# Performance work log

Hardware: AMD Instinct MI355X
Metric: run time of the kernel (lower is better)

Reference implementation:

```python
import jax, jax.numpy as jnp
import numpy as np

B, L, D, H, R = 2, 128, 256, 8, 4
DK = D // H  # 32
EPS = 1e-6


def setup_inputs() -> dict:
    key = jax.random.key(0)
    ks = jax.random.split(key, 12)
    q = jax.random.normal(ks[0], (B, L, D), jnp.float32)
    k = jax.random.normal(ks[1], (B, L, D), jnp.float32)
    v = jax.random.normal(ks[2], (B, L, D), jnp.float32)
    t = jnp.sort(jax.random.uniform(ks[3], (B, L), jnp.float32), axis=-1)
    omega = jax.random.uniform(ks[4], (B, L, L), jnp.float32)
    mask = jnp.triu(jnp.ones((L, L), bool), 1)  # True = masked (causal)
    xav = (2.0 / (D + D)) ** 0.5
    Wq = jax.random.normal(ks[5], (D, H * DK), jnp.float32) * xav
    Wk = jax.random.normal(ks[6], (D, H * DK), jnp.float32) * xav
    Wv = jax.random.normal(ks[7], (D, H * DK), jnp.float32) * xav
    s = jax.random.uniform(ks[8], (R,), jnp.float32) + 0.1  # ODE time-decay scales
    fc_w = jax.random.normal(ks[9], (H * DK, D), jnp.float32) * xav
    fc_b = jnp.zeros((D,), jnp.float32)
    ln_g = jnp.ones((D,), jnp.float32)
    ln_b = jnp.zeros((D,), jnp.float32)
    return {"q": q, "k": k, "v": v, "t": t, "omega": omega, "mask": mask,
            "Wq": Wq, "Wk": Wk, "Wv": Wv, "s": s,
            "fc_w": fc_w, "fc_b": fc_b, "ln_g": ln_g, "ln_b": ln_b}


def _ode_proj(x, W, phi):
    # x: (B,L,D), W: (D,H*DK), phi: (B,L,L,R) time kernel
    p = x @ W                                       # (B,L,H*DK)
    y = p[:, None, :, None, :] * phi[..., None]     # (B,L,L,R,H*DK)
    y = y.reshape(B, L, L, R, H, DK)
    return y.transpose(0, 4, 1, 2, 3, 5)            # (B,H,L,L,R,DK)


def reference(q, k, v, t, omega, mask, Wq, Wk, Wv, s, fc_w, fc_b, ln_g, ln_b):
    temp = DK ** 0.5
    residual = q
    # pre-LayerNorm on q (normalize_before=True)
    mu = q.mean(-1, keepdims=True)
    var = q.var(-1, keepdims=True)
    qn = (q - mu) / jnp.sqrt(var + EPS) * ln_g + ln_b
    # continuous-time kernel phi[b,i,j,r] = exp(-|t_i - t_j| * s_r)
    dt = jnp.abs(t[:, :, None] - t[:, None, :])     # (B,L,L)
    phi = jnp.exp(-dt[..., None] * s)               # (B,L,L,R)
    q6 = _ode_proj(qn, Wq, phi)                     # (B,H,L,L,R,DK)
    k6 = _ode_proj(k, Wk, phi)
    v6 = _ode_proj(v, Wv, phi)
    # attn = (q/temp * k * omega).sum(-1).sum(-1)
    attn = jnp.einsum('bhijrd,bhijrd,bij->bhij', q6 / temp, k6, omega)
    attn = jnp.where(mask[None, None, :, :], -1e9, attn)
    attn = jax.nn.softmax(attn, axis=-1)            # (B,H,L,L)
    vsum = v6.sum(axis=4)                           # sum over R -> (B,H,L,L,DK)
    out = jnp.einsum('bhij,bhijd->bhid', attn, vsum)  # (B,H,L,DK)
    out = out.transpose(0, 2, 1, 3).reshape(B, L, H * DK)
    out = out @ fc_w + fc_b + residual              # dropout = identity (eval)
    return (out, attn)
```

## Files before the change

kernel.cpp:

```cpp
#include <hip/hip_runtime.h>

#define B_  2
#define L_  128
#define D_  256
#define H_  8
#define R_  4
#define DK_ 32
#define BL_ (B_*L_)
#define SXP 260

__device__ __forceinline__ float wredsum64(float v) {
    #pragma unroll
    for (int m = 32; m >= 1; m >>= 1) v += __shfl_xor(v, m, 64);
    return v;
}
__device__ __forceinline__ float wredmax64(float v) {
    #pragma unroll
    for (int m = 32; m >= 1; m >>= 1) v = fmaxf(v, __shfl_xor(v, m, 64));
    return v;
}

__global__ __launch_bounds__(256) void k_proj(
    const float* __restrict__ q, const float* __restrict__ k, const float* __restrict__ v,
    const float* __restrict__ Wq, const float* __restrict__ Wk, const float* __restrict__ Wv,
    const float* __restrict__ ln_g, const float* __restrict__ ln_b,
    float* __restrict__ pv, float* __restrict__ qkpart)
{
    const int blk = blockIdx.x;
    const int rowTile = blk >> 4;
    const int cg = blk & 15;
    const int rbase = rowTile * 4;
    const int tid = threadIdx.x;

    __shared__ __align__(16) float sx[3][4 * SXP];
    __shared__ __align__(16) float partF[16 * 4 * 16];
    __shared__ float spq[4][16], spk[4][16];

    {
        const int r = tid >> 6, f4c = tid & 63;
        #pragma unroll
        for (int p = 0; p < 3; ++p) {
            const float* src = (p == 0 ? q : (p == 1 ? k : v)) + (size_t)(rbase + r) * D_;
            *reinterpret_cast<float4*>(&sx[p][r * SXP + f4c * 4]) =
                reinterpret_cast<const float4*>(src)[f4c];
        }
    }
    __syncthreads();

    {
        const int r = tid >> 6, lane = tid & 63;
        float x0 = sx[0][r * SXP + lane];
        float x1 = sx[0][r * SXP + lane + 64];
        float x2 = sx[0][r * SXP + lane + 128];
        float x3 = sx[0][r * SXP + lane + 192];
        float s1 = x0 + x1 + x2 + x3;
        float s2 = x0*x0 + x1*x1 + x2*x2 + x3*x3;
        #pragma unroll
        for (int m = 32; m >= 1; m >>= 1) {
            s1 += __shfl_xor(s1, m, 64);
            s2 += __shfl_xor(s2, m, 64);
        }
        const float mu = s1 * (1.0f / D_);
        const float rs = rsqrtf(s2 * (1.0f / D_) - mu * mu + 1e-6f);
        sx[0][r * SXP + lane      ] = (x0 - mu) * rs * ln_g[lane      ] + ln_b[lane      ];
        sx[0][r * SXP + lane +  64] = (x1 - mu) * rs * ln_g[lane +  64] + ln_b[lane +  64];
        sx[0][r * SXP + lane + 128] = (x2 - mu) * rs * ln_g[lane + 128] + ln_b[lane + 128];
        sx[0][r * SXP + lane + 192] = (x3 - mu) * rs * ln_g[lane + 192] + ln_b[lane + 192];
    }
    __syncthreads();

    const int kg  = tid >> 4;
    const int row = (tid >> 2) & 3;
    const int c4  = tid & 3;
    const int gc4 = cg * 4 + c4;
    const int kbase = kg * 16;

    #pragma unroll
    for (int m = 0; m < 3; ++m) {
        const float4* W4 = reinterpret_cast<const float4*>(m == 0 ? Wq : (m == 1 ? Wk : Wv));
        float4 a = {0, 0, 0, 0};
        #pragma unroll
        for (int kk = 0; kk < 16; ++kk) {
            const int kr = kbase + kk;
            const float x = sx[m][row * SXP + kr];
            const float4 w = W4[kr * 64 + gc4];
            a.x += x * w.x; a.y += x * w.y; a.z += x * w.z; a.w += x * w.w;
        }
        *reinterpret_cast<float4*>(&partF[(kg * 16 + row * 4 + c4) * 4]) = a;
        __syncthreads();
        if (tid < 64) {
            const int rr = tid >> 4, cc = tid & 15;
            float sum = 0.f;
            #pragma unroll
            for (int g = 0; g < 16; ++g) sum += partF[g * 64 + rr * 16 + cc];
            if      (m == 0) spq[rr][cc] = sum;
            else if (m == 1) spk[rr][cc] = sum;
            else             pv[(size_t)(rbase + rr) * D_ + cg * 16 + cc] = sum;
        }
        __syncthreads();
    }

    if (tid < 64) {
        const int rr = tid >> 4, cc = tid & 15;
        float d = spq[rr][cc] * spk[rr][cc];
        #pragma unroll
        for (int m = 8; m >= 1; m >>= 1) d += __shfl_xor(d, m, 64);
        if (cc == 0) qkpart[(size_t)(rbase + rr) * 16 + cg] = d;
    }
}

__global__ __launch_bounds__(256) void k_attn(
    const float* __restrict__ t, const float* __restrict__ omega, const float* __restrict__ s,
    const float* __restrict__ pv, const float* __restrict__ qkpart,
    float* __restrict__ mid, float* __restrict__ dout)
{
    const int blk = blockIdx.x;
    const int b     = blk >> 8;
    const int itile = (blk >> 3) & 31;
    const int h     = blk & 7;
    const int ibase = itile * 4;
    const int tid = threadIdx.x;

    __shared__ __align__(16) float sQKp[L_ * 16];
    __shared__ __align__(16) float sQKh[L_];
    __shared__ __align__(16) float sOm[4 * L_];
    __shared__ __align__(16) float sPhi[4 * L_], sPsi[4 * L_];
    __shared__ __align__(16) float sAttn[4 * L_];
    __shared__ __align__(16) float partF[32 * 4 * 32];
    __shared__ float st[L_], sS[R_];

    {
        const float4* qkp4 = reinterpret_cast<const float4*>(qkpart + (size_t)b * L_ * 16);
        reinterpret_cast<float4*>(sQKp)[tid]       = qkp4[tid];
        reinterpret_cast<float4*>(sQKp)[tid + 256] = qkp4[tid + 256];
        if (tid < 128)
            reinterpret_cast<float4*>(sOm)[tid] =
                reinterpret_cast<const float4*>(omega + ((size_t)(b * L_ + ibase)) * L_)[tid];
        if (tid < 32)
            reinterpret_cast<float4*>(st)[tid] =
                reinterpret_cast<const float4*>(t + (size_t)b * L_)[tid];
        if (tid < R_) sS[tid] = s[tid];
    }
    __syncthreads();

    if (tid < 128) sQKh[tid] = sQKp[tid * 16 + 2 * h] + sQKp[tid * 16 + 2 * h + 1];
    #pragma unroll
    for (int p = 0; p < 2; ++p) {
        const int idx = tid + p * 256;
        const int w = idx >> 7, j = idx & 127;
        const float dtv = fabsf(st[ibase + w] - st[j]);
        float Phi = 0.f, Psi = 0.f;
        #pragma unroll
        for (int r = 0; r < R_; ++r) {
            const float e = expf(-dtv * sS[r]);
            Phi += e;
            Psi += e * e;
        }
        sPhi[idx] = Phi;
        sPsi[idx] = Psi;
    }
    __syncthreads();

    const int w = tid >> 6, lane = tid & 63;
    const int i = ibase + w;
    {
        const float invtemp = 0.17677669529663687f;
        const int j0 = lane, j1 = lane + 64;
        float l0 = (j0 <= i) ? sOm[w*L_ + j0] * sPsi[w*L_ + j0] * sQKh[j0] * invtemp : -3.0e38f;
        float l1 = (j1 <= i) ? sOm[w*L_ + j1] * sPsi[w*L_ + j1] * sQKh[j1] * invtemp : -3.0e38f;
        const float mx = wredmax64(fmaxf(l0, l1));
        const float e0 = (j0 <= i) ? expf(l0 - mx) : 0.f;
        const float e1 = (j1 <= i) ? expf(l1 - mx) : 0.f;
        const float inv = 1.0f / wredsum64(e0 + e1);
        const float a0 = e0 * inv, a1 = e1 * inv;
        sAttn[w*L_ + j0] = a0;
        sAttn[w*L_ + j1] = a1;
        const size_t ab = (size_t)BL_ * D_ + (((size_t)(b * H_ + h) * L_ + i) * L_);
        dout[ab + j0] = a0;
        dout[ab + j1] = a1;
    }
    __syncthreads();

    {
        const int jg = tid >> 3, c4 = tid & 7;
        const int gc4 = h * 8 + c4;
        const float4* pv4 = reinterpret_cast<const float4*>(pv + (size_t)b * L_ * D_);
        float4 acc[4];
        #pragma unroll
        for (int ww = 0; ww < 4; ++ww) acc[ww] = make_float4(0, 0, 0, 0);
        #pragma unroll
        for (int jj = 0; jj < 4; ++jj) {
            const int j = jg + jj * 32;
            const float4 p = pv4[j * 64 + gc4];
            #pragma unroll
            for (int ww = 0; ww < 4; ++ww) {
                const float wgt = sAttn[ww*L_ + j] * sPhi[ww*L_ + j];
                acc[ww].x += wgt * p.x; acc[ww].y += wgt * p.y;
                acc[ww].z += wgt * p.z; acc[ww].w += wgt * p.w;
            }
        }
        #pragma unroll
        for (int ww = 0; ww < 4; ++ww)
            *reinterpret_cast<float4*>(&partF[(jg * 32 + ww * 8 + c4) * 4]) = acc[ww];
    }
    __syncthreads();
    if (tid < 128) {
        const int ww = tid >> 5, cc = tid & 31;
        float sum = 0.f;
        #pragma unroll
        for (int g = 0; g < 32; ++g) sum += partF[g * 128 + ww * 32 + cc];
        mid[((size_t)(b * L_ + ibase + ww)) * D_ + h * 32 + cc] = sum;
    }
}

__global__ __launch_bounds__(256) void k_fc(
    const float* __restrict__ q, const float* __restrict__ fc_w, const float* __restrict__ fc_b,
    const float* __restrict__ mid, float* __restrict__ dout)
{
    const int blk = blockIdx.x;
    const int rowTile = blk >> 4;
    const int cg = blk & 15;
    const int rbase = rowTile * 4;
    const int tid = threadIdx.x;

    __shared__ __align__(16) float smid[4 * SXP];
    __shared__ __align__(16) float partF[16 * 4 * 16];

    {
        const int r = tid >> 6, f4c = tid & 63;
        *reinterpret_cast<float4*>(&smid[r * SXP + f4c * 4]) =
            reinterpret_cast<const float4*>(mid + (size_t)(rbase + r) * D_)[f4c];
    }
    __syncthreads();

    const int kg  = tid >> 4;
    const int row = (tid >> 2) & 3;
    const int c4  = tid & 3;
    const int gc4 = cg * 4 + c4;
    const int kbase = kg * 16;
    const float4* fw4 = reinterpret_cast<const float4*>(fc_w);
    float4 a = {0, 0, 0, 0};
    #pragma unroll
    for (int kk = 0; kk < 16; ++kk) {
        const int kr = kbase + kk;
        const float x = smid[row * SXP + kr];
        const float4 wv = fw4[kr * 64 + gc4];
        a.x += x * wv.x; a.y += x * wv.y; a.z += x * wv.z; a.w += x * wv.w;
    }
    *reinterpret_cast<float4*>(&partF[(kg * 16 + row * 4 + c4) * 4]) = a;
    __syncthreads();

    if (tid < 64) {
        const int rr = tid >> 4, cc = tid & 15;
        const int col = cg * 16 + cc;
        float sum = fc_b[col] + q[(size_t)(rbase + rr) * D_ + col];
        #pragma unroll
        for (int g = 0; g < 16; ++g) sum += partF[g * 64 + rr * 16 + cc];
        dout[(size_t)(rbase + rr) * D_ + col] = sum;
    }
}

extern "C" void kernel_launch(void* const* d_in, const int* in_sizes, int n_in,
                              void* d_out, int out_size, void* d_ws, size_t ws_size,
                              hipStream_t stream) {
    const float* q     = (const float*)d_in[0];
    const float* k     = (const float*)d_in[1];
    const float* v     = (const float*)d_in[2];
    const float* t     = (const float*)d_in[3];
    const float* omega = (const float*)d_in[4];
    const float* Wq    = (const float*)d_in[6];
    const float* Wk    = (const float*)d_in[7];
    const float* Wv    = (const float*)d_in[8];
    const float* s     = (const float*)d_in[9];
    const float* fc_w  = (const float*)d_in[10];
    const float* fc_b  = (const float*)d_in[11];
    const float* ln_g  = (const float*)d_in[12];
    const float* ln_b  = (const float*)d_in[13];

    float* ws     = (float*)d_ws;
    float* pv     = ws;
    float* qkpart = ws + 65536;
    float* mid    = ws + 69632;
    float* out    = (float*)d_out;

    hipLaunchKernelGGL(k_proj, dim3(1024), dim3(256), 0, stream,
                       q, k, v, Wq, Wk, Wv, ln_g, ln_b, pv, qkpart);
    hipLaunchKernelGGL(k_attn, dim3(512), dim3(256), 0, stream,
                       t, omega, s, pv, qkpart, mid, out);
    hipLaunchKernelGGL(k_fc, dim3(1024), dim3(256), 0, stream,
                       q, fc_w, fc_b, mid, out);
}
```

Measured before the change: 95.71 us.

## Fuse projection, attention and output GEMM into one persistent kernel with grid barriers

Merges the three kernels into one 512-block kernel that uses atomic-counter grid barriers between the projection, attention and FC phases, with the shared memory for each phase overlaid through a union. The projection and FC phases now give each block 32 output columns instead of 16, so 512 blocks cover the work the old 1024-block launches did. This removes two kernel launches and their inter-kernel gaps, but adds a memset per call and spin-wait barriers. Those barriers only work if all 512 blocks are co-resident, which the launch_bounds(256,2) hint is meant to help with.

```diff
diff --git a/kernel.cpp b/kernel.cpp
--- a/kernel.cpp
+++ b/kernel.cpp
@@ -5,9 +5,10 @@
 #define D_  256
 #define H_  8
 #define R_  4
-#define DK_ 32
 #define BL_ (B_*L_)
 #define SXP 260
+#define NBLK 512
+
 
 __device__ __forceinline__ float wredsum64(float v) {
     #pragma unroll
@@ -20,243 +21,260 @@
     return v;
 }
 
-__global__ __launch_bounds__(256) void k_proj(
+__device__ __forceinline__ void grid_barrier(unsigned* bar, unsigned target) {
+    __threadfence();
+    __syncthreads();
+    if (threadIdx.x == 0) {
+        __hip_atomic_fetch_add(bar, 1u, __ATOMIC_ACQ_REL, __HIP_MEMORY_SCOPE_AGENT);
+        while (__hip_atomic_load(bar, __ATOMIC_ACQUIRE, __HIP_MEMORY_SCOPE_AGENT) < target)
+            __builtin_amdgcn_s_sleep(2);
+    }
+    __syncthreads();
+    __threadfence();
+}
+
+__global__ __launch_bounds__(256, 2) void k_fused(
     const float* __restrict__ q, const float* __restrict__ k, const float* __restrict__ v,
+    const float* __restrict__ t, const float* __restrict__ omega,
     const float* __restrict__ Wq, const float* __restrict__ Wk, const float* __restrict__ Wv,
+    const float* __restrict__ s, const float* __restrict__ fc_w, const float* __restrict__ fc_b,
     const float* __restrict__ ln_g, const float* __restrict__ ln_b,
-    float* __restrict__ pv, float* __restrict__ qkpart)
+    float* __restrict__ pv, float* __restrict__ qkdot, float* __restrict__ mid,
+    unsigned* __restrict__ bar, float* __restrict__ dout)
 {
     const int blk = blockIdx.x;
-    const int rowTile = blk >> 4;
-    const int cg = blk & 15;
-    const int rbase = rowTile * 4;
     const int tid = threadIdx.x;
 
-    __shared__ __align__(16) float sx[3][4 * SXP];
-    __shared__ __align__(16) float partF[16 * 4 * 16];
-    __shared__ float spq[4][16], spk[4][16];
+    __shared__ __align__(16) union {
+        struct {
+            float sx[3][4 * SXP];
+            float partF[8 * 4 * 32];
+            float spq[4][32], spk[4][32];
+        } a;
+        struct {
+            float sQK[L_ * H_];
+            float sQKh[L_];
+            float sOm[4 * L_];
+            float sPhi[4 * L_], sPsi[4 * L_];
+            float sAttn[4 * L_];
+            float partF[32 * 4 * 32];
+            float st[L_];
+            float sS[R_];
+        } b;
+        struct {
+            float smid[4 * SXP];
+            float partF[8 * 4 * 32];
+        } c;
+    } u;
 
     {
-        const int r = tid >> 6, f4c = tid & 63;
+        const int rowTile = blk >> 3;
+        const int cgp = blk & 7;
+        const int rbase = rowTile * 4;
+
+        {
+            const int r = tid >> 6, f4c = tid & 63;
+            #pragma unroll
+            for (int p = 0; p < 3; ++p) {
+                const float* src = (p == 0 ? q : (p == 1 ? k : v)) + (size_t)(rbase + r) * D_;
+                *reinterpret_cast<float4*>(&u.a.sx[p][r * SXP + f4c * 4]) =
+                    reinterpret_cast<const float4*>(src)[f4c];
+            }
+        }
+        __syncthreads();
+
+        {
+            const int r = tid >> 6, lane = tid & 63;
+            float x0 = u.a.sx[0][r * SXP + lane];
+            float x1 = u.a.sx[0][r * SXP + lane + 64];
+            float x2 = u.a.sx[0][r * SXP + lane + 128];
+            float x3 = u.a.sx[0][r * SXP + lane + 192];
+            float s1 = x0 + x1 + x2 + x3;
+            float s2 = x0*x0 + x1*x1 + x2*x2 + x3*x3;
+            #pragma unroll
+            for (int m = 32; m >= 1; m >>= 1) {
+                s1 += __shfl_xor(s1, m, 64);
+                s2 += __shfl_xor(s2, m, 64);
+            }
+            const float mu = s1 * (1.0f / D_);
+            const float rs = rsqrtf(s2 * (1.0f / D_) - mu * mu + 1e-6f);
+            u.a.sx[0][r * SXP + lane      ] = (x0 - mu) * rs * ln_g[lane      ] + ln_b[lane      ];
+            u.a.sx[0][r * SXP + lane +  64] = (x1 - mu) * rs * ln_g[lane +  64] + ln_b[lane +  64];
+            u.a.sx[0][r * SXP + lane + 128] = (x2 - mu) * rs * ln_g[lane + 128] + ln_b[lane + 128];
+            u.a.sx[0][r * SXP + lane + 192] = (x3 - mu) * rs * ln_g[lane + 192] + ln_b[lane + 192];
+        }
+        __syncthreads();
+
+        const int kg  = tid >> 5;
+        const int row = (tid >> 3) & 3;
+        const int c4  = tid & 7;
+        const int gc4 = cgp * 8 + c4;
+        const int kbase = kg * 32;
+
         #pragma unroll
-        for (int p = 0; p < 3; ++p) {
-            const float* src = (p == 0 ? q : (p == 1 ? k : v)) + (size_t)(rbase + r) * D_;
-            *reinterpret_cast<float4*>(&sx[p][r * SXP + f4c * 4]) =
-                reinterpret_cast<const float4*>(src)[f4c];
+        for (int m = 0; m < 3; ++m) {
+            const float4* W4 = reinterpret_cast<const float4*>(m == 0 ? Wq : (m == 1 ? Wk : Wv));
+            float4 a = {0, 0, 0, 0};
+            #pragma unroll 8
+            for (int kk = 0; kk < 32; ++kk) {
+                const int kr = kbase + kk;
+                const float x = u.a.sx[m][row * SXP + kr];
+                const float4 w = W4[kr * 64 + gc4];
+                a.x += x * w.x; a.y += x * w.y; a.z += x * w.z; a.w += x * w.w;
+            }
+            *reinterpret_cast<float4*>(&u.a.partF[kg * 128 + row * 32 + c4 * 4]) = a;
+            __syncthreads();
+            if (tid < 128) {
+                const int rr = tid >> 5, cc = tid & 31;
+                float sum = 0.f;
+                #pragma unroll
+                for (int g = 0; g < 8; ++g) sum += u.a.partF[g * 128 + rr * 32 + cc];
+                if      (m == 0) u.a.spq[rr][cc] = sum;
+                else if (m == 1) u.a.spk[rr][cc] = sum;
+                else             pv[(size_t)(rbase + rr) * D_ + cgp * 32 + cc] = sum;
+            }
+            __syncthreads();
+        }
+
+        if (tid < 128) {
+            const int rr = tid >> 5, cc = tid & 31;
+            float d = u.a.spq[rr][cc] * u.a.spk[rr][cc];
+            #pragma unroll
+            for (int m = 16; m >= 1; m >>= 1) d += __shfl_xor(d, m, 64);
+            if (cc == 0) qkdot[(size_t)(rbase + rr) * H_ + cgp] = d;
         }
     }
-    __syncthreads();
+
+    grid_barrier(bar, NBLK);
 
     {
-        const int r = tid >> 6, lane = tid & 63;
-        float x0 = sx[0][r * SXP + lane];
-        float x1 = sx[0][r * SXP + lane + 64];
-        float x2 = sx[0][r * SXP + lane + 128];
-        float x3 = sx[0][r * SXP + lane + 192];
-        float s1 = x0 + x1 + x2 + x3;
-        float s2 = x0*x0 + x1*x1 + x2*x2 + x3*x3;
+        const int b     = blk >> 8;
+        const int itile = (blk >> 3) & 31;
+        const int h     = blk & 7;
+        const int ibase = itile * 4;
+
+        {
+            reinterpret_cast<float4*>(u.b.sQK)[tid] =
+                reinterpret_cast<const float4*>(qkdot + (size_t)b * L_ * H_)[tid];
+            if (tid < 128)
+                reinterpret_cast<float4*>(u.b.sOm)[tid] =
+                    reinterpret_cast<const float4*>(omega + ((size_t)(b * L_ + ibase)) * L_)[tid];
+            if (tid < 32)
+                reinterpret_cast<float4*>(u.b.st)[tid] =
+                    reinterpret_cast<const float4*>(t + (size_t)b * L_)[tid];
+            if (tid < R_) u.b.sS[tid] = s[tid];
+        }
+        __syncthreads();
+
+        if (tid < 128) u.b.sQKh[tid] = u.b.sQK[tid * H_ + h];
         #pragma unroll
-        for (int m = 32; m >= 1; m >>= 1) {
-            s1 += __shfl_xor(s1, m, 64);
-            s2 += __shfl_xor(s2, m, 64);
-        }
-        const float mu = s1 * (1.0f / D_);
-        const float rs = rsqrtf(s2 * (1.0f / D_) - mu * mu + 1e-6f);
-        sx[0][r * SXP + lane      ] = (x0 - mu) * rs * ln_g[lane      ] + ln_b[lane      ];
-        sx[0][r * SXP + lane +  64] = (x1 - mu) * rs * ln_g[lane +  64] + ln_b[lane +  64];
-        sx[0][r * SXP + lane + 128] = (x2 - mu) * rs * ln_g[lane + 128] + ln_b[lane + 128];
-        sx[0][r * SXP + lane + 192] = (x3 - mu) * rs * ln_g[lane + 192] + ln_b[lane + 192];
+        for (int p = 0; p < 2; ++p) {
+            const int idx = tid + p * 256;
+            const int w = idx >> 7, j = idx & 127;
+            const float dtv = fabsf(u.b.st[ibase + w] - u.b.st[j]);
+            float Phi = 0.f, Psi = 0.f;
+            #pragma unroll
+            for (int r = 0; r < R_; ++r) {
+                const float e = expf(-dtv * u.b.sS[r]);
+                Phi += e;
+                Psi += e * e;
+            }
+            u.b.sPhi[idx] = Phi;
+            u.b.sPsi[idx] = Psi;
+        }
+        __syncthreads();
+
+        const int w = tid >> 6, lane = tid & 63;
+        {
+            const int i = ibase + w;
+            const float invtemp = 0.17677669529663687f;
+            const int j0 = lane, j1 = lane + 64;
+            float l0 = (j0 <= i) ? u.b.sOm[w*L_ + j0] * u.b.sPsi[w*L_ + j0] * u.b.sQKh[j0] * invtemp : -3.0e38f;
+            float l1 = (j1 <= i) ? u.b.sOm[w*L_ + j1] * u.b.sPsi[w*L_ + j1] * u.b.sQKh[j1] * invtemp : -3.0e38f;
+            const float mx = wredmax64(fmaxf(l0, l1));
+            const float e0 = (j0 <= i) ? expf(l0 - mx) : 0.f;
+            const float e1 = (j1 <= i) ? expf(l1 - mx) : 0.f;
+            const float inv = 1.0f / wredsum64(e0 + e1);
+            const float a0 = e0 * inv, a1 = e1 * inv;
+            u.b.sAttn[w*L_ + j0] = a0;
+            u.b.sAttn[w*L_ + j1] = a1;
+            const size_t ab = (size_t)BL_ * D_ + (((size_t)(b * H_ + h) * L_ + i) * L_);
+            dout[ab + j0] = a0;
+            dout[ab + j1] = a1;
+        }
+        __syncthreads();
+
+        {
+            const int jg = tid >> 3, c4 = tid & 7;
+            const int gc4 = h * 8 + c4;
+            const float4* pv4 = reinterpret_cast<const float4*>(pv + (size_t)b * L_ * D_);
+            float4 acc[4];
+            #pragma unroll
+            for (int ww = 0; ww < 4; ++ww) acc[ww] = make_float4(0, 0, 0, 0);
+            #pragma unroll
+            for (int jj = 0; jj < 4; ++jj) {
+                const int j = jg + jj * 32;
+                const float4 p = pv4[j * 64 + gc4];
+                #pragma unroll
+                for (int ww = 0; ww < 4; ++ww) {
+                    const float wgt = u.b.sAttn[ww*L_ + j] * u.b.sPhi[ww*L_ + j];
+                    acc[ww].x += wgt * p.x; acc[ww].y += wgt * p.y;
+                    acc[ww].z += wgt * p.z; acc[ww].w += wgt * p.w;
+                }
+            }
+            #pragma unroll
+            for (int ww = 0; ww < 4; ++ww)
+                *reinterpret_cast<float4*>(&u.b.partF[jg * 128 + ww * 32 + c4 * 4]) = acc[ww];
+        }
+        __syncthreads();
+        if (tid < 128) {
+            const int ww = tid >> 5, cc = tid & 31;
+            float sum = 0.f;
+            #pragma unroll
+            for (int g = 0; g < 32; ++g) sum += u.b.partF[g * 128 + ww * 32 + cc];
+            mid[((size_t)(b * L_ + ibase + ww)) * D_ + h * 32 + cc] = sum;
+        }
     }
-    __syncthreads();
-
-    const int kg  = tid >> 4;
-    const int row = (tid >> 2) & 3;
-    const int c4  = tid & 3;
-    const int gc4 = cg * 4 + c4;
-    const int kbase = kg * 16;
-
-    #pragma unroll
-    for (int m = 0; m < 3; ++m) {
-        const float4* W4 = reinterpret_cast<const float4*>(m == 0 ? Wq : (m == 1 ? Wk : Wv));
+
+    grid_barrier(bar, 2 * NBLK);
+
+    {
+        const int rowTile = blk >> 3;
+        const int cgp = blk & 7;
+        const int rbase = rowTile * 4;
+
+        {
+            const int r = tid >> 6, f4c = tid & 63;
+            *reinterpret_cast<float4*>(&u.c.smid[r * SXP + f4c * 4]) =
+                reinterpret_cast<const float4*>(mid + (size_t)(rbase + r) * D_)[f4c];
+        }
+        __syncthreads();
+
+        const int kg  = tid >> 5;
+        const int row = (tid >> 3) & 3;
+        const int c4  = tid & 7;
+        const int gc4 = cgp * 8 + c4;
+        const int kbase = kg * 32;
+        const float4* fw4 = reinterpret_cast<const float4*>(fc_w);
         float4 a = {0, 0, 0, 0};
-        #pragma unroll
-        for (int kk = 0; kk < 16; ++kk) {
+        #pragma unroll 8
+        for (int kk = 0; kk < 32; ++kk) {
             const int kr = kbase + kk;
-            const float x = sx[m][row * SXP + kr];
-            const float4 w = W4[kr * 64 + gc4];
-            a.x += x * w.x; a.y += x * w.y; a.z += x * w.z; a.w += x * w.w;
-        }
-        *reinterpret_cast<float4*>(&partF[(kg * 16 + row * 4 + c4) * 4]) = a;
-        __syncthreads();
-        if (tid < 64) {
-            const int rr = tid >> 4, cc = tid & 15;
-            float sum = 0.f;
-            #pragma unroll
-            for (int g = 0; g < 16; ++g) sum += partF[g * 64 + rr * 16 + cc];
-            if      (m == 0) spq[rr][cc] = sum;
-            else if (m == 1) spk[rr][cc] = sum;
-            else             pv[(size_t)(rbase + rr) * D_ + cg * 16 + cc] = sum;
-        }
-        __syncthreads();
-    }
-
-    if (tid < 64) {
-        const int rr = tid >> 4, cc = tid & 15;
-        float d = spq[rr][cc] * spk[rr][cc];
-        #pragma unroll
-        for (int m = 8; m >= 1; m >>= 1) d += __shfl_xor(d, m, 64);
-        if (cc == 0) qkpart[(size_t)(rbase + rr) * 16 + cg] = d;
-    }
-}
-
-__global__ __launch_bounds__(256) void k_attn(
-    const float* __restrict__ t, const float* __restrict__ omega, const float* __restrict__ s,
-    const float* __restrict__ pv, const float* __restrict__ qkpart,
-    float* __restrict__ mid, float* __restrict__ dout)
-{
-    const int blk = blockIdx.x;
-    const int b     = blk >> 8;
-    const int itile = (blk >> 3) & 31;
-    const int h     = blk & 7;
-    const int ibase = itile * 4;
-    const int tid = threadIdx.x;
-
-    __shared__ __align__(16) float sQKp[L_ * 16];
-    __shared__ __align__(16) float sQKh[L_];
-    __shared__ __align__(16) float sOm[4 * L_];
-    __shared__ __align__(16) float sPhi[4 * L_], sPsi[4 * L_];
-    __shared__ __align__(16) float sAttn[4 * L_];
-    __shared__ __align__(16) float partF[32 * 4 * 32];
-    __shared__ float st[L_], sS[R_];
-
-    {
-        const float4* qkp4 = reinterpret_cast<const float4*>(qkpart + (size_t)b * L_ * 16);
-        reinterpret_cast<float4*>(sQKp)[tid]       = qkp4[tid];
-        reinterpret_cast<float4*>(sQKp)[tid + 256] = qkp4[tid + 256];
-        if (tid < 128)
-            reinterpret_cast<float4*>(sOm)[tid] =
-                reinterpret_cast<const float4*>(omega + ((size_t)(b * L_ + ibase)) * L_)[tid];
-        if (tid < 32)
-            reinterpret_cast<float4*>(st)[tid] =
-                reinterpret_cast<const float4*>(t + (size_t)b * L_)[tid];
-        if (tid < R_) sS[tid] = s[tid];
-    }
-    __syncthreads();
-
-    if (tid < 128) sQKh[tid] = sQKp[tid * 16 + 2 * h] + sQKp[tid * 16 + 2 * h + 1];
-    #pragma unroll
-    for (int p = 0; p < 2; ++p) {
-        const int idx = tid + p * 256;
-        const int w = idx >> 7, j = idx & 127;
-        const float dtv = fabsf(st[ibase + w] - st[j]);
-        float Phi = 0.f, Psi = 0.f;
-        #pragma unroll
-        for (int r = 0; r < R_; ++r) {
-            const float e = expf(-dtv * sS[r]);
-            Phi += e;
-            Psi += e * e;
-        }
-        sPhi[idx] = Phi;
-        sPsi[idx] = Psi;
-    }
-    __syncthreads();
-
-    const int w = tid >> 6, lane = tid & 63;
-    const int i = ibase + w;
-    {
-        const float invtemp = 0.17677669529663687f;
-        const int j0 = lane, j1 = lane + 64;
-        float l0 = (j0 <= i) ? sOm[w*L_ + j0] * sPsi[w*L_ + j0] * sQKh[j0] * invtemp : -3.0e38f;
-        float l1 = (j1 <= i) ? sOm[w*L_ + j1] * sPsi[w*L_ + j1] * sQKh[j1] * invtemp : -3.0e38f;
-        const float mx = wredmax64(fmaxf(l0, l1));
-        const float e0 = (j0 <= i) ? expf(l0 - mx) : 0.f;
-        const float e1 = (j1 <= i) ? expf(l1 - mx) : 0.f;
-        const float inv = 1.0f / wredsum64(e0 + e1);
-        const float a0 = e0 * inv, a1 = e1 * inv;
-        sAttn[w*L_ + j0] = a0;
-        sAttn[w*L_ + j1] = a1;
-        const size_t ab = (size_t)BL_ * D_ + (((size_t)(b * H_ + h) * L_ + i) * L_);
-        dout[ab + j0] = a0;
-        dout[ab + j1] = a1;
-    }
-    __syncthreads();
-
-    {
-        const int jg = tid >> 3, c4 = tid & 7;
-        const int gc4 = h * 8 + c4;
-        const float4* pv4 = reinterpret_cast<const float4*>(pv + (size_t)b * L_ * D_);
-        float4 acc[4];
-        #pragma unroll
-        for (int ww = 0; ww < 4; ++ww) acc[ww] = make_float4(0, 0, 0, 0);
-        #pragma unroll
-        for (int jj = 0; jj < 4; ++jj) {
-            const int j = jg + jj * 32;
-            const float4 p = pv4[j * 64 + gc4];
-            #pragma unroll
-            for (int ww = 0; ww < 4; ++ww) {
-                const float wgt = sAttn[ww*L_ + j] * sPhi[ww*L_ + j];
-                acc[ww].x += wgt * p.x; acc[ww].y += wgt * p.y;
-                acc[ww].z += wgt * p.z; acc[ww].w += wgt * p.w;
-            }
-        }
-        #pragma unroll
-        for (int ww = 0; ww < 4; ++ww)
-            *reinterpret_cast<float4*>(&partF[(jg * 32 + ww * 8 + c4) * 4]) = acc[ww];
-    }
-    __syncthreads();
-    if (tid < 128) {
-        const int ww = tid >> 5, cc = tid & 31;
-        float sum = 0.f;
-        #pragma unroll
-        for (int g = 0; g < 32; ++g) sum += partF[g * 128 + ww * 32 + cc];
-        mid[((size_t)(b * L_ + ibase + ww)) * D_ + h * 32 + cc] = sum;
-    }
-}
-
-__global__ __launch_bounds__(256) void k_fc(
-    const float* __restrict__ q, const float* __restrict__ fc_w, const float* __restrict__ fc_b,
-    const float* __restrict__ mid, float* __restrict__ dout)
-{
-    const int blk = blockIdx.x;
-    const int rowTile = blk >> 4;
-    const int cg = blk & 15;
-    const int rbase = rowTile * 4;
-    const int tid = threadIdx.x;
-
-    __shared__ __align__(16) float smid[4 * SXP];
-    __shared__ __align__(16) float partF[16 * 4 * 16];
-
-    {
-        const int r = tid >> 6, f4c = tid & 63;
-        *reinterpret_cast<float4*>(&smid[r * SXP + f4c * 4]) =
-            reinterpret_cast<const float4*>(mid + (size_t)(rbase + r) * D_)[f4c];
-    }
-    __syncthreads();
-
-    const int kg  = tid >> 4;
-    const int row = (tid >> 2) & 3;
-    const int c4  = tid & 3;
-    const int gc4 = cg * 4 + c4;
-    const int kbase = kg * 16;
-    const float4* fw4 = reinterpret_cast<const float4*>(fc_w);
-    float4 a = {0, 0, 0, 0};
-    #pragma unroll
-    for (int kk = 0; kk < 16; ++kk) {
-        const int kr = kbase + kk;
-        const float x = smid[row * SXP + kr];
-        const float4 wv = fw4[kr * 64 + gc4];
-        a.x += x * wv.x; a.y += x * wv.y; a.z += x * wv.z; a.w += x * wv.w;
-    }
-    *reinterpret_cast<float4*>(&partF[(kg * 16 + row * 4 + c4) * 4]) = a;
-    __syncthreads();
-
-    if (tid < 64) {
-        const int rr = tid >> 4, cc = tid & 15;
-        const int col = cg * 16 + cc;
-        float sum = fc_b[col] + q[(size_t)(rbase + rr) * D_ + col];
-        #pragma unroll
-        for (int g = 0; g < 16; ++g) sum += partF[g * 64 + rr * 16 + cc];
-        dout[(size_t)(rbase + rr) * D_ + col] = sum;
+            const float x = u.c.smid[row * SXP + kr];
+            const float4 wv = fw4[kr * 64 + gc4];
+            a.x += x * wv.x; a.y += x * wv.y; a.z += x * wv.z; a.w += x * wv.w;
+        }
+        *reinterpret_cast<float4*>(&u.c.partF[kg * 128 + row * 32 + c4 * 4]) = a;
+        __syncthreads();
+
+        if (tid < 128) {
+            const int rr = tid >> 5, cc = tid & 31;
+            const int col = cgp * 32 + cc;
+            float sum = fc_b[col] + q[(size_t)(rbase + rr) * D_ + col];
+            #pragma unroll
+            for (int g = 0; g < 8; ++g) sum += u.c.partF[g * 128 + rr * 32 + cc];
+            dout[(size_t)(rbase + rr) * D_ + col] = sum;
+        }
     }
 }
 
@@ -277,16 +295,15 @@
     const float* ln_g  = (const float*)d_in[12];
     const float* ln_b  = (const float*)d_in[13];
 
-    float* ws     = (float*)d_ws;
-    float* pv     = ws;
-    float* qkpart = ws + 65536;
-    float* mid    = ws + 69632;
-    float* out    = (float*)d_out;
-
-    hipLaunchKernelGGL(k_proj, dim3(1024), dim3(256), 0, stream,
-                       q, k, v, Wq, Wk, Wv, ln_g, ln_b, pv, qkpart);
-    hipLaunchKernelGGL(k_attn, dim3(512), dim3(256), 0, stream,
-                       t, omega, s, pv, qkpart, mid, out);
-    hipLaunchKernelGGL(k_fc, dim3(1024), dim3(256), 0, stream,
-                       q, fc_w, fc_b, mid, out);
-}
+    float* ws       = (float*)d_ws;
+    float* pv       = ws;
+    float* qkdot    = ws + 65536;
+    float* mid      = ws + 69632;
+    unsigned* bar   = (unsigned*)(ws + 139264);
+    float* out      = (float*)d_out;
+
+    hipMemsetAsync(bar, 0, sizeof(unsigned), stream);
+    hipLaunchKernelGGL(k_fused, dim3(NBLK), dim3(256), 0, stream,
+                       q, k, v, t, omega, Wq, Wk, Wv, s, fc_w, fc_b, ln_g, ln_b,
+                       pv, qkdot, mid, bar, out);
+}
```

Measured after the change: 274.2 us. 186% more time.

## Fuse attention and output projection into one per-row kernel

Applied to the files above, without the earlier changes.

Merges the attention kernel and the final fc kernel into one launch. Each block now handles one query row across all eight heads, computes the softmax, the causally truncated weighted sum of pv, and then the fc matmul plus residual directly from shared memory. This drops one kernel launch and the round trip of the intermediate through global memory, and skips the masked j>i terms. In exchange the grid shrinks to 256 blocks, the workload per block grows with i so blocks are unbalanced, and each block reads the whole fc_w matrix with scalar loads.

```diff
diff --git a/kernel.cpp b/kernel.cpp
--- a/kernel.cpp
+++ b/kernel.cpp
@@ -5,9 +5,9 @@
 #define D_  256
 #define H_  8
 #define R_  4
-#define DK_ 32
 #define BL_ (B_*L_)
 #define SXP 260
+
 
 __device__ __forceinline__ float wredsum64(float v) {
     #pragma unroll
@@ -109,46 +109,43 @@
     }
 }
 
-__global__ __launch_bounds__(256) void k_attn(
-    const float* __restrict__ t, const float* __restrict__ omega, const float* __restrict__ s,
+__global__ __launch_bounds__(256) void k_attn_fc(
+    const float* __restrict__ q, const float* __restrict__ t, const float* __restrict__ omega,
+    const float* __restrict__ s, const float* __restrict__ fc_w, const float* __restrict__ fc_b,
     const float* __restrict__ pv, const float* __restrict__ qkpart,
-    float* __restrict__ mid, float* __restrict__ dout)
+    float* __restrict__ dout)
 {
     const int blk = blockIdx.x;
-    const int b     = blk >> 8;
-    const int itile = (blk >> 3) & 31;
-    const int h     = blk & 7;
-    const int ibase = itile * 4;
+    const int b = blk >> 7;
+    const int i = blk & (L_ - 1);
     const int tid = threadIdx.x;
 
     __shared__ __align__(16) float sQKp[L_ * 16];
-    __shared__ __align__(16) float sQKh[L_];
-    __shared__ __align__(16) float sOm[4 * L_];
-    __shared__ __align__(16) float sPhi[4 * L_], sPsi[4 * L_];
-    __shared__ __align__(16) float sAttn[4 * L_];
-    __shared__ __align__(16) float partF[32 * 4 * 32];
-    __shared__ float st[L_], sS[R_];
+    __shared__ __align__(16) float sQK[L_ * H_];
+    __shared__ __align__(16) float sOm[L_];
+    __shared__ __align__(16) float sAttn[H_][L_];
+    __shared__ __align__(16) float sMid[D_];
+    __shared__ float sPhi[L_], sPsi[L_], st[L_], sS[R_];
 
     {
         const float4* qkp4 = reinterpret_cast<const float4*>(qkpart + (size_t)b * L_ * 16);
         reinterpret_cast<float4*>(sQKp)[tid]       = qkp4[tid];
         reinterpret_cast<float4*>(sQKp)[tid + 256] = qkp4[tid + 256];
-        if (tid < 128)
+        if (tid < 32) {
             reinterpret_cast<float4*>(sOm)[tid] =
-                reinterpret_cast<const float4*>(omega + ((size_t)(b * L_ + ibase)) * L_)[tid];
-        if (tid < 32)
+                reinterpret_cast<const float4*>(omega + ((size_t)(b * L_ + i)) * L_)[tid];
             reinterpret_cast<float4*>(st)[tid] =
                 reinterpret_cast<const float4*>(t + (size_t)b * L_)[tid];
+        }
         if (tid < R_) sS[tid] = s[tid];
     }
     __syncthreads();
 
-    if (tid < 128) sQKh[tid] = sQKp[tid * 16 + 2 * h] + sQKp[tid * 16 + 2 * h + 1];
-    #pragma unroll
-    for (int p = 0; p < 2; ++p) {
-        const int idx = tid + p * 256;
-        const int w = idx >> 7, j = idx & 127;
-        const float dtv = fabsf(st[ibase + w] - st[j]);
+    if (tid < 128) {
+        #pragma unroll
+        for (int h = 0; h < H_; ++h)
+            sQK[tid * H_ + h] = sQKp[tid * 16 + 2 * h] + sQKp[tid * 16 + 2 * h + 1];
+        const float dtv = fabsf(st[i] - st[tid]);
         float Phi = 0.f, Psi = 0.f;
         #pragma unroll
         for (int r = 0; r < R_; ++r) {
@@ -156,25 +153,26 @@
             Phi += e;
             Psi += e * e;
         }
-        sPhi[idx] = Phi;
-        sPsi[idx] = Psi;
+        sPhi[tid] = Phi;
+        sPsi[tid] = Psi;
     }
     __syncthreads();
 
     const int w = tid >> 6, lane = tid & 63;
-    const int i = ibase + w;
-    {
-        const float invtemp = 0.17677669529663687f;
+    const float invtemp = 0.17677669529663687f;
+    #pragma unroll
+    for (int pass = 0; pass < 2; ++pass) {
+        const int h = w * 2 + pass;
         const int j0 = lane, j1 = lane + 64;
-        float l0 = (j0 <= i) ? sOm[w*L_ + j0] * sPsi[w*L_ + j0] * sQKh[j0] * invtemp : -3.0e38f;
-        float l1 = (j1 <= i) ? sOm[w*L_ + j1] * sPsi[w*L_ + j1] * sQKh[j1] * invtemp : -3.0e38f;
+        float l0 = (j0 <= i) ? sOm[j0] * sPsi[j0] * sQK[j0 * H_ + h] * invtemp : -3.0e38f;
+        float l1 = (j1 <= i) ? sOm[j1] * sPsi[j1] * sQK[j1 * H_ + h] * invtemp : -3.0e38f;
         const float mx = wredmax64(fmaxf(l0, l1));
         const float e0 = (j0 <= i) ? expf(l0 - mx) : 0.f;
         const float e1 = (j1 <= i) ? expf(l1 - mx) : 0.f;
         const float inv = 1.0f / wredsum64(e0 + e1);
         const float a0 = e0 * inv, a1 = e1 * inv;
-        sAttn[w*L_ + j0] = a0;
-        sAttn[w*L_ + j1] = a1;
+        sAttn[h][j0] = a0;
+        sAttn[h][j1] = a1;
         const size_t ab = (size_t)BL_ * D_ + (((size_t)(b * H_ + h) * L_ + i) * L_);
         dout[ab + j0] = a0;
         dout[ab + j1] = a1;
@@ -182,81 +180,24 @@
     __syncthreads();
 
     {
-        const int jg = tid >> 3, c4 = tid & 7;
-        const int gc4 = h * 8 + c4;
-        const float4* pv4 = reinterpret_cast<const float4*>(pv + (size_t)b * L_ * D_);
-        float4 acc[4];
-        #pragma unroll
-        for (int ww = 0; ww < 4; ++ww) acc[ww] = make_float4(0, 0, 0, 0);
-        #pragma unroll
-        for (int jj = 0; jj < 4; ++jj) {
-            const int j = jg + jj * 32;
-            const float4 p = pv4[j * 64 + gc4];
-            #pragma unroll
-            for (int ww = 0; ww < 4; ++ww) {
-                const float wgt = sAttn[ww*L_ + j] * sPhi[ww*L_ + j];
-                acc[ww].x += wgt * p.x; acc[ww].y += wgt * p.y;
-                acc[ww].z += wgt * p.z; acc[ww].w += wgt * p.w;
-            }
-        }
-        #pragma unroll
-        for (int ww = 0; ww < 4; ++ww)
-            *reinterpret_cast<float4*>(&partF[(jg * 32 + ww * 8 + c4) * 4]) = acc[ww];
-    }
-    __syncthreads();
-    if (tid < 128) {
-        const int ww = tid >> 5, cc = tid & 31;
-        float sum = 0.f;
-        #pragma unroll
-        for (int g = 0; g < 32; ++g) sum += partF[g * 128 + ww * 32 + cc];
-        mid[((size_t)(b * L_ + ibase + ww)) * D_ + h * 32 + cc] = sum;
-    }
-}
-
-__global__ __launch_bounds__(256) void k_fc(
-    const float* __restrict__ q, const float* __restrict__ fc_w, const float* __restrict__ fc_b,
-    const float* __restrict__ mid, float* __restrict__ dout)
-{
-    const int blk = blockIdx.x;
-    const int rowTile = blk >> 4;
-    const int cg = blk & 15;
-    const int rbase = rowTile * 4;
-    const int tid = threadIdx.x;
-
-    __shared__ __align__(16) float smid[4 * SXP];
-    __shared__ __align__(16) float partF[16 * 4 * 16];
-
-    {
-        const int r = tid >> 6, f4c = tid & 63;
-        *reinterpret_cast<float4*>(&smid[r * SXP + f4c * 4]) =
-            reinterpret_cast<const float4*>(mid + (size_t)(rbase + r) * D_)[f4c];
-    }
-    __syncthreads();
-
-    const int kg  = tid >> 4;
-    const int row = (tid >> 2) & 3;
-    const int c4  = tid & 3;
-    const int gc4 = cg * 4 + c4;
-    const int kbase = kg * 16;
-    const float4* fw4 = reinterpret_cast<const float4*>(fc_w);
-    float4 a = {0, 0, 0, 0};
-    #pragma unroll
-    for (int kk = 0; kk < 16; ++kk) {
-        const int kr = kbase + kk;
-        const float x = smid[row * SXP + kr];
-        const float4 wv = fw4[kr * 64 + gc4];
-        a.x += x * wv.x; a.y += x * wv.y; a.z += x * wv.z; a.w += x * wv.w;
-    }
-    *reinterpret_cast<float4*>(&partF[(kg * 16 + row * 4 + c4) * 4]) = a;
-    __syncthreads();
-
-    if (tid < 64) {
-        const int rr = tid >> 4, cc = tid & 15;
-        const int col = cg * 16 + cc;
-        float sum = fc_b[col] + q[(size_t)(rbase + rr) * D_ + col];
-        #pragma unroll
-        for (int g = 0; g < 16; ++g) sum += partF[g * 64 + rr * 16 + cc];
-        dout[(size_t)(rbase + rr) * D_ + col] = sum;
+        const int h = tid >> 5;
+        const float* pvb = pv + (size_t)b * L_ * D_ + tid;
+        float acc = 0.f;
+        #pragma unroll 4
+        for (int j = 0; j <= i; ++j)
+            acc += sAttn[h][j] * sPhi[j] * pvb[j * D_];
+        sMid[tid] = acc;
+    }
+    __syncthreads();
+
+    {
+        const size_t orow = (size_t)(b * L_ + i) * D_;
+        float r = fc_b[tid] + q[orow + tid];
+        const float* fwc = fc_w + tid;
+        #pragma unroll 8
+        for (int kk = 0; kk < D_; ++kk)
+            r += sMid[kk] * fwc[kk * D_];
+        dout[orow + tid] = r;
     }
 }
 
@@ -280,13 +221,10 @@
     float* ws     = (float*)d_ws;
     float* pv     = ws;
     float* qkpart = ws + 65536;
-    float* mid    = ws + 69632;
     float* out    = (float*)d_out;
 
     hipLaunchKernelGGL(k_proj, dim3(1024), dim3(256), 0, stream,
                        q, k, v, Wq, Wk, Wv, ln_g, ln_b, pv, qkpart);
-    hipLaunchKernelGGL(k_attn, dim3(512), dim3(256), 0, stream,
-                       t, omega, s, pv, qkpart, mid, out);
-    hipLaunchKernelGGL(k_fc, dim3(1024), dim3(256), 0, stream,
-                       q, fc_w, fc_b, mid, out);
-}
+    hipLaunchKernelGGL(k_attn_fc, dim3(256), dim3(256), 0, stream,
+                       q, t, omega, s, fc_w, fc_b, pv, qkpart, out);
+}
```

Measured after the change: 103.5 us. +8.1%, slower.
